# Optimization experiments

Measured on AMD Instinct MI355X. Metric: run time of the kernel, lower is better.

Reference implementation:

```python
import jax, jax.numpy as jnp
import numpy as np

N_NODES = 100000
N_EDGES = 1000000
NODE_DIM = 128
EDGE_DIM = 16
HID = 128


def _linear_init(key, fan_in, fan_out):
    # torch nn.Linear default: U(-1/sqrt(fan_in), 1/sqrt(fan_in))
    kw, kb = jax.random.split(key)
    bound = 1.0 / np.sqrt(fan_in)
    W = jax.random.uniform(kw, (fan_in, fan_out), jnp.float32, -bound, bound)
    b = jax.random.uniform(kb, (fan_out,), jnp.float32, -bound, bound)
    return W, b


def setup_inputs() -> dict:
    key = jax.random.key(0)
    ks = jax.random.split(key, 12)
    node_features = jax.random.normal(ks[0], (N_NODES, NODE_DIM), jnp.float32)
    edge_index = jax.random.randint(ks[1], (2, N_EDGES), 0, N_NODES, jnp.int64 if jax.config.read('jax_enable_x64') else jnp.int32)
    edge_features = jax.random.normal(ks[2], (N_EDGES, EDGE_DIM), jnp.float32)
    Wn1, bn1 = _linear_init(ks[3], NODE_DIM, HID)
    Wn2, bn2 = _linear_init(ks[4], HID, HID)
    We1, be1 = _linear_init(ks[5], EDGE_DIM, HID)
    We2, be2 = _linear_init(ks[6], HID, HID)
    Wp1, bp1 = _linear_init(ks[7], HID * 3, HID)
    Wp2, bp2 = _linear_init(ks[8], HID, HID // 2)
    Wp3, bp3 = _linear_init(ks[9], HID // 2, 1)
    return dict(node_features=node_features, edge_index=edge_index, edge_features=edge_features,
                Wn1=Wn1, bn1=bn1, Wn2=Wn2, bn2=bn2,
                We1=We1, be1=be1, We2=We2, be2=be2,
                Wp1=Wp1, bp1=bp1, Wp2=Wp2, bp2=bp2, Wp3=Wp3, bp3=bp3)


def reference(node_features, edge_index, edge_features,
              Wn1, bn1, Wn2, bn2, We1, be1, We2, be2,
              Wp1, bp1, Wp2, bp2, Wp3, bp3):
    # node/edge encoders: Linear -> ReLU -> Linear
    node_emb = jax.nn.relu(node_features @ Wn1 + bn1) @ Wn2 + bn2  # [N, H]
    edge_emb = jax.nn.relu(edge_features @ We1 + be1) @ We2 + be2  # [E, H]
    src = node_emb[edge_index[0]]  # [E, H] gather
    dst = node_emb[edge_index[1]]  # [E, H] gather
    combined = jnp.concatenate([src, dst, edge_emb], axis=1)  # [E, 3H]
    # predictor MLP (Dropout(0.2) is identity at inference)
    h = jax.nn.relu(combined @ Wp1 + bp1)
    h = jax.nn.relu(h @ Wp2 + bp2)
    scores = jax.nn.sigmoid(h @ Wp3 + bp3)  # [E, 1]
    return scores
```

## Files before the change

kernel.cpp:

```cpp
#include <hip/hip_runtime.h>

typedef _Float16 f16;
typedef _Float16 f16x8 __attribute__((ext_vector_type(8)));
typedef float    f32x4 __attribute__((ext_vector_type(4)));
typedef f16x8 f16x8_a __attribute__((may_alias));
typedef f16   f16_a   __attribute__((may_alias));

#define NN 100000
#define NE 1000000

static __device__ __forceinline__ f32x4 mfma16(f16x8 a, f16x8 b, f32x4 c) {
  return __builtin_amdgcn_mfma_f32_16x16x32_f16(a, b, c, 0, 0, 0);
}

static __device__ __forceinline__ f16x8 zero8() {
  f16x8 z; 
#pragma unroll
  for (int j = 0; j < 8; ++j) z[j] = (f16)0.f;
  return z;
}

template<int RB_LOG2, int SZ>
static __device__ __forceinline__ void load_weights(const f16* __restrict__ gw, char* lds) {
  const char* src = (const char*)gw;
#pragma unroll
  for (int g = threadIdx.x; g < SZ / 16; g += 256) {
    int byte = g << 4;
    int row  = byte >> RB_LOG2;
    int dstb = byte ^ ((row & 7) << 4);
    f16x8 v = *(const f16x8_a*)(src + byte);
    *(f16x8_a*)(lds + dstb) = v;
  }
}

template<int RB_LOG2>
static __device__ __forceinline__ f16x8 read_b(const char* lds, int n, int kbyte) {
  int byte = ((n << RB_LOG2) + kbyte) ^ ((n & 7) << 4);
  return *(const f16x8_a*)(lds + byte);
}

static __device__ __forceinline__ f16x8 act_read(const char* act, int base, int m, int kbyte) {
  int byte = (base + m * 256 + kbyte) ^ ((m & 7) << 4);
  return *(const f16x8_a*)(act + byte);
}

static __device__ __forceinline__ void act_write(char* act, int base, int m, int col, f16 v) {
  int byte = (base + m * 256 + col * 2) ^ ((m & 7) << 4);
  *(f16_a*)(act + byte) = v;
}

__global__ void transpose_w(const float* __restrict__ src, f16* __restrict__ dst,
                            int K, int N, int kOff, int ld) {
  int i = blockIdx.x * 256 + threadIdx.x;
  if (i >= N * K) return;
  int n = i / K, k = i - n * K;
  dst[i] = (f16)src[(size_t)(kOff + k) * ld + n];
}

__global__ __launch_bounds__(256, 2) void node_kernel(
    const float* __restrict__ nf, const f16* __restrict__ WnT1, const float* __restrict__ bn1,
    const f16* __restrict__ WnT2, const float* __restrict__ bn2, f16* __restrict__ emb) {
  __shared__ char wbuf[32768];
  __shared__ char act[32768];
  const int tid = threadIdx.x, w = tid >> 6, lane = tid & 63;
  const int c = lane & 15, kb = lane >> 4;
  const int base = blockIdx.x * 128 + w * 32;
  const int abase = w * 8192;

  load_weights<8, 32768>(WnT1, wbuf);
  __syncthreads();

  f16x8 a[2][4];
#pragma unroll
  for (int rt = 0; rt < 2; ++rt) {
    int r = base + rt * 16 + c; r = r < NN ? r : 0;
    const float* p = nf + (size_t)r * 128 + kb * 8;
#pragma unroll
    for (int ks = 0; ks < 4; ++ks) {
      float4 x0 = *(const float4*)(p + ks * 32);
      float4 x1 = *(const float4*)(p + ks * 32 + 4);
      f16x8 t;
      t[0]=(f16)x0.x; t[1]=(f16)x0.y; t[2]=(f16)x0.z; t[3]=(f16)x0.w;
      t[4]=(f16)x1.x; t[5]=(f16)x1.y; t[6]=(f16)x1.z; t[7]=(f16)x1.w;
      a[rt][ks] = t;
    }
  }

  f32x4 acc[2][8];
#pragma unroll
  for (int nt = 0; nt < 8; ++nt) {
    float bb = bn1[nt * 16 + c];
    acc[0][nt] = f32x4{bb, bb, bb, bb};
    acc[1][nt] = f32x4{bb, bb, bb, bb};
  }
#pragma unroll
  for (int ks = 0; ks < 4; ++ks)
#pragma unroll
    for (int nt = 0; nt < 8; ++nt) {
      f16x8 b = read_b<8>(wbuf, nt * 16 + c, ks * 64 + kb * 16);
      acc[0][nt] = mfma16(a[0][ks], b, acc[0][nt]);
      acc[1][nt] = mfma16(a[1][ks], b, acc[1][nt]);
    }
#pragma unroll
  for (int rt = 0; rt < 2; ++rt)
#pragma unroll
    for (int nt = 0; nt < 8; ++nt)
#pragma unroll
      for (int r = 0; r < 4; ++r) {
        float v = acc[rt][nt][r];
        v = v > 0.f ? v : 0.f;
        act_write(act, abase, rt * 16 + kb * 4 + r, nt * 16 + c, (f16)v);
      }

  __syncthreads();
  load_weights<8, 32768>(WnT2, wbuf);
  __syncthreads();

  f32x4 acc2[2][8];
#pragma unroll
  for (int nt = 0; nt < 8; ++nt) {
    float bb = bn2[nt * 16 + c];
    acc2[0][nt] = f32x4{bb, bb, bb, bb};
    acc2[1][nt] = f32x4{bb, bb, bb, bb};
  }
#pragma unroll
  for (int ks = 0; ks < 4; ++ks) {
    f16x8 a0 = act_read(act, abase, c,      ks * 64 + kb * 16);
    f16x8 a1 = act_read(act, abase, 16 + c, ks * 64 + kb * 16);
#pragma unroll
    for (int nt = 0; nt < 8; ++nt) {
      f16x8 b = read_b<8>(wbuf, nt * 16 + c, ks * 64 + kb * 16);
      acc2[0][nt] = mfma16(a0, b, acc2[0][nt]);
      acc2[1][nt] = mfma16(a1, b, acc2[1][nt]);
    }
  }
#pragma unroll
  for (int rt = 0; rt < 2; ++rt)
#pragma unroll
    for (int nt = 0; nt < 8; ++nt)
#pragma unroll
      for (int r = 0; r < 4; ++r) {
        int row = base + rt * 16 + kb * 4 + r;
        if (row < NN) emb[(size_t)row * 128 + nt * 16 + c] = (f16)acc2[rt][nt][r];
      }
}

__global__ __launch_bounds__(256, 2) void edge_kernel(
    const float* __restrict__ ef, const int* __restrict__ eidx,
    const f16* __restrict__ emb,
    const f16* __restrict__ WeT1, const float* __restrict__ be1,
    const f16* __restrict__ WeT2, const float* __restrict__ be2,
    const f16* __restrict__ Wp1a, const f16* __restrict__ Wp1b, const f16* __restrict__ Wp1c,
    const float* __restrict__ bp1,
    const f16* __restrict__ WpT2, const float* __restrict__ bp2,
    const float* __restrict__ Wp3, const float* __restrict__ bp3,
    float* __restrict__ out) {
  __shared__ char wbuf[32768];
  __shared__ char act[32768];
  const int tid = threadIdx.x, w = tid >> 6, lane = tid & 63;
  const int c = lane & 15, kb = lane >> 4;
  const int ebase = blockIdx.x * 128 + w * 32;
  const int abase = w * 8192;

  load_weights<5, 4096>(WeT1, wbuf);
  __syncthreads();
  {
    f16x8 a[2];
#pragma unroll
    for (int rt = 0; rt < 2; ++rt) {
      int m = ebase + rt * 16 + c; m = m < NE ? m : 0;
      f16x8 t = zero8();
      if (kb < 2) {
        const float* p = ef + (size_t)m * 16 + kb * 8;
        float4 x0 = *(const float4*)(p);
        float4 x1 = *(const float4*)(p + 4);
        t[0]=(f16)x0.x; t[1]=(f16)x0.y; t[2]=(f16)x0.z; t[3]=(f16)x0.w;
        t[4]=(f16)x1.x; t[5]=(f16)x1.y; t[6]=(f16)x1.z; t[7]=(f16)x1.w;
      }
      a[rt] = t;
    }
    f32x4 acc[2][8];
#pragma unroll
    for (int nt = 0; nt < 8; ++nt) {
      float bb = be1[nt * 16 + c];
      acc[0][nt] = f32x4{bb, bb, bb, bb};
      acc[1][nt] = f32x4{bb, bb, bb, bb};
    }
    int kbyte = (kb < 2) ? kb * 16 : 0;
#pragma unroll
    for (int nt = 0; nt < 8; ++nt) {
      f16x8 b = read_b<5>(wbuf, nt * 16 + c, kbyte);
      acc[0][nt] = mfma16(a[0], b, acc[0][nt]);
      acc[1][nt] = mfma16(a[1], b, acc[1][nt]);
    }
#pragma unroll
    for (int rt = 0; rt < 2; ++rt)
#pragma unroll
      for (int nt = 0; nt < 8; ++nt)
#pragma unroll
        for (int r = 0; r < 4; ++r) {
          float v = acc[rt][nt][r];
          v = v > 0.f ? v : 0.f;
          act_write(act, abase, rt * 16 + kb * 4 + r, nt * 16 + c, (f16)v);
        }
  }

  __syncthreads();
  load_weights<8, 32768>(WeT2, wbuf);
  __syncthreads();
  {
    f32x4 acc[2][8];
#pragma unroll
    for (int nt = 0; nt < 8; ++nt) {
      float bb = be2[nt * 16 + c];
      acc[0][nt] = f32x4{bb, bb, bb, bb};
      acc[1][nt] = f32x4{bb, bb, bb, bb};
    }
#pragma unroll
    for (int ks = 0; ks < 4; ++ks) {
      f16x8 a0 = act_read(act, abase, c,      ks * 64 + kb * 16);
      f16x8 a1 = act_read(act, abase, 16 + c, ks * 64 + kb * 16);
#pragma unroll
      for (int nt = 0; nt < 8; ++nt) {
        f16x8 b = read_b<8>(wbuf, nt * 16 + c, ks * 64 + kb * 16);
        acc[0][nt] = mfma16(a0, b, acc[0][nt]);
        acc[1][nt] = mfma16(a1, b, acc[1][nt]);
      }
    }
#pragma unroll
    for (int rt = 0; rt < 2; ++rt)
#pragma unroll
      for (int nt = 0; nt < 8; ++nt)
#pragma unroll
        for (int r = 0; r < 4; ++r)
          act_write(act, abase, rt * 16 + kb * 4 + r, nt * 16 + c, (f16)acc[rt][nt][r]);
  }

  f32x4 accp[2][8];
#pragma unroll
  for (int nt = 0; nt < 8; ++nt) {
    float bb = bp1[nt * 16 + c];
    accp[0][nt] = f32x4{bb, bb, bb, bb};
    accp[1][nt] = f32x4{bb, bb, bb, bb};
  }

  __syncthreads();
  load_weights<8, 32768>(Wp1a, wbuf);
  __syncthreads();
  {
    f16x8 a[2][4];
#pragma unroll
    for (int rt = 0; rt < 2; ++rt) {
      int m = ebase + rt * 16 + c; m = m < NE ? m : NE - 1;
      int s = eidx[m];
      const f16* np = emb + (size_t)s * 128 + kb * 8;
#pragma unroll
      for (int ks = 0; ks < 4; ++ks) a[rt][ks] = *(const f16x8_a*)(np + ks * 32);
    }
#pragma unroll
    for (int ks = 0; ks < 4; ++ks)
#pragma unroll
      for (int nt = 0; nt < 8; ++nt) {
        f16x8 b = read_b<8>(wbuf, nt * 16 + c, ks * 64 + kb * 16);
        accp[0][nt] = mfma16(a[0][ks], b, accp[0][nt]);
        accp[1][nt] = mfma16(a[1][ks], b, accp[1][nt]);
      }
  }

  __syncthreads();
  load_weights<8, 32768>(Wp1b, wbuf);
  __syncthreads();
  {
    f16x8 a[2][4];
#pragma unroll
    for (int rt = 0; rt < 2; ++rt) {
      int m = ebase + rt * 16 + c; m = m < NE ? m : NE - 1;
      int s = eidx[NE + m];
      const f16* np = emb + (size_t)s * 128 + kb * 8;
#pragma unroll
      for (int ks = 0; ks < 4; ++ks) a[rt][ks] = *(const f16x8_a*)(np + ks * 32);
    }
#pragma unroll
    for (int ks = 0; ks < 4; ++ks)
#pragma unroll
      for (int nt = 0; nt < 8; ++nt) {
        f16x8 b = read_b<8>(wbuf, nt * 16 + c, ks * 64 + kb * 16);
        accp[0][nt] = mfma16(a[0][ks], b, accp[0][nt]);
        accp[1][nt] = mfma16(a[1][ks], b, accp[1][nt]);
      }
  }

  __syncthreads();
  load_weights<8, 32768>(Wp1c, wbuf);
  __syncthreads();
  {
#pragma unroll
    for (int ks = 0; ks < 4; ++ks) {
      f16x8 a0 = act_read(act, abase, c,      ks * 64 + kb * 16);
      f16x8 a1 = act_read(act, abase, 16 + c, ks * 64 + kb * 16);
#pragma unroll
      for (int nt = 0; nt < 8; ++nt) {
        f16x8 b = read_b<8>(wbuf, nt * 16 + c, ks * 64 + kb * 16);
        accp[0][nt] = mfma16(a0, b, accp[0][nt]);
        accp[1][nt] = mfma16(a1, b, accp[1][nt]);
      }
    }
#pragma unroll
    for (int rt = 0; rt < 2; ++rt)
#pragma unroll
      for (int nt = 0; nt < 8; ++nt)
#pragma unroll
        for (int r = 0; r < 4; ++r) {
          float v = accp[rt][nt][r];
          v = v > 0.f ? v : 0.f;
          act_write(act, abase, rt * 16 + kb * 4 + r, nt * 16 + c, (f16)v);
        }
  }

  __syncthreads();
  load_weights<8, 16384>(WpT2, wbuf);
  __syncthreads();
  f32x4 accq[2][4];
#pragma unroll
  for (int nt = 0; nt < 4; ++nt) {
    float bb = bp2[nt * 16 + c];
    accq[0][nt] = f32x4{bb, bb, bb, bb};
    accq[1][nt] = f32x4{bb, bb, bb, bb};
  }
#pragma unroll
  for (int ks = 0; ks < 4; ++ks) {
    f16x8 a0 = act_read(act, abase, c,      ks * 64 + kb * 16);
    f16x8 a1 = act_read(act, abase, 16 + c, ks * 64 + kb * 16);
#pragma unroll
    for (int nt = 0; nt < 4; ++nt) {
      f16x8 b = read_b<8>(wbuf, nt * 16 + c, ks * 64 + kb * 16);
      accq[0][nt] = mfma16(a0, b, accq[0][nt]);
      accq[1][nt] = mfma16(a1, b, accq[1][nt]);
    }
  }

  float w3[4], b3 = bp3[0];
#pragma unroll
  for (int nt = 0; nt < 4; ++nt) w3[nt] = Wp3[nt * 16 + c];
#pragma unroll
  for (int rt = 0; rt < 2; ++rt) {
#pragma unroll
    for (int r = 0; r < 4; ++r) {
      float s = 0.f;
#pragma unroll
      for (int nt = 0; nt < 4; ++nt) {
        float h = accq[rt][nt][r];
        h = h > 0.f ? h : 0.f;
        s += h * w3[nt];
      }
      s += __shfl_xor(s, 1, 64);
      s += __shfl_xor(s, 2, 64);
      s += __shfl_xor(s, 4, 64);
      s += __shfl_xor(s, 8, 64);
      int m = ebase + rt * 16 + kb * 4 + r;
      if (c == r && m < NE) {
        out[m] = 1.f / (1.f + __expf(-(s + b3)));
      }
    }
  }
}

extern "C" void kernel_launch(void* const* d_in, const int* in_sizes, int n_in,
                              void* d_out, int out_size, void* d_ws, size_t ws_size,
                              hipStream_t stream) {
  const float* nf  = (const float*)d_in[0];
  const int*   ei  = (const int*)  d_in[1];
  const float* ef  = (const float*)d_in[2];
  const float* Wn1 = (const float*)d_in[3];
  const float* bn1 = (const float*)d_in[4];
  const float* Wn2 = (const float*)d_in[5];
  const float* bn2 = (const float*)d_in[6];
  const float* We1 = (const float*)d_in[7];
  const float* be1 = (const float*)d_in[8];
  const float* We2 = (const float*)d_in[9];
  const float* be2 = (const float*)d_in[10];
  const float* Wp1 = (const float*)d_in[11];
  const float* bp1 = (const float*)d_in[12];
  const float* Wp2 = (const float*)d_in[13];
  const float* bp2 = (const float*)d_in[14];
  const float* Wp3 = (const float*)d_in[15];
  const float* bp3 = (const float*)d_in[16];

  char* ws = (char*)d_ws;
  f16* WnT1 = (f16*)(ws);
  f16* WnT2 = (f16*)(ws + 32768);
  f16* WeT1 = (f16*)(ws + 65536);
  f16* WeT2 = (f16*)(ws + 69632);
  f16* Wp1a = (f16*)(ws + 102400);
  f16* Wp1b = (f16*)(ws + 135168);
  f16* Wp1c = (f16*)(ws + 167936);
  f16* WpT2 = (f16*)(ws + 200704);
  f16* emb  = (f16*)(ws + 217088);

  transpose_w<<<64, 256, 0, stream>>>(Wn1, WnT1, 128, 128, 0, 128);
  transpose_w<<<64, 256, 0, stream>>>(Wn2, WnT2, 128, 128, 0, 128);
  transpose_w<<<8,  256, 0, stream>>>(We1, WeT1, 16,  128, 0, 128);
  transpose_w<<<64, 256, 0, stream>>>(We2, WeT2, 128, 128, 0, 128);
  transpose_w<<<64, 256, 0, stream>>>(Wp1, Wp1a, 128, 128, 0,   128);
  transpose_w<<<64, 256, 0, stream>>>(Wp1, Wp1b, 128, 128, 128, 128);
  transpose_w<<<64, 256, 0, stream>>>(Wp1, Wp1c, 128, 128, 256, 128);
  transpose_w<<<32, 256, 0, stream>>>(Wp2, WpT2, 128, 64, 0, 64);

  node_kernel<<<782, 256, 0, stream>>>(nf, WnT1, bn1, WnT2, bn2, emb);
  edge_kernel<<<7813, 256, 0, stream>>>(ef, ei, emb, WeT1, be1, WeT2, be2,
                                        Wp1a, Wp1b, Wp1c, bp1, WpT2, bp2, Wp3, bp3,
                                        (float*)d_out);
}
```

Baseline: 485.1 us.

## Fold second-layer weights into predictor and precompute per-node projections

```diff
diff --git a/kernel.cpp b/kernel.cpp
--- a/kernel.cpp
+++ b/kernel.cpp
@@ -8,16 +8,26 @@
 
 #define NN 100000
 #define NE 1000000
+#define NT 31250
+#define EK_BLOCKS 512
+#define EK_WAVES (EK_BLOCKS * 4)
 
 static __device__ __forceinline__ f32x4 mfma16(f16x8 a, f16x8 b, f32x4 c) {
   return __builtin_amdgcn_mfma_f32_16x16x32_f16(a, b, c, 0, 0, 0);
 }
 
 static __device__ __forceinline__ f16x8 zero8() {
-  f16x8 z; 
+  f16x8 z;
 #pragma unroll
   for (int j = 0; j < 8; ++j) z[j] = (f16)0.f;
   return z;
+}
+
+static __device__ __forceinline__ f16x8 relu8(f16x8 x) {
+  f16x8 r;
+#pragma unroll
+  for (int j = 0; j < 8; ++j) r[j] = x[j] > (f16)0.f ? x[j] : (f16)0.f;
+  return r;
 }
 
 template<int RB_LOG2, int SZ>
@@ -57,9 +67,34 @@
   dst[i] = (f16)src[(size_t)(kOff + k) * ld + n];
 }
 
+__global__ void mm_fold(const float* __restrict__ A, const float* __restrict__ Wp1,
+                        int rowOff, f16* __restrict__ dstT) {
+  int g = blockIdx.x * 256 + threadIdx.x;
+  int i = g >> 7, j = g & 127;
+  float s = 0.f;
+#pragma unroll 8
+  for (int k = 0; k < 128; ++k) s += A[i * 128 + k] * Wp1[(size_t)(rowOff + k) * 128 + j];
+  dstT[j * 128 + i] = (f16)s;
+}
+
+__global__ void bias_fold(const float* __restrict__ bp1, const float* __restrict__ bn2,
+                          const float* __restrict__ be2, const float* __restrict__ Wp1,
+                          float* __restrict__ bfold) {
+  int j = threadIdx.x;
+  float s = bp1[j];
+#pragma unroll 8
+  for (int k = 0; k < 128; ++k)
+    s += bn2[k] * (Wp1[(size_t)k * 128 + j] + Wp1[(size_t)(128 + k) * 128 + j]);
+#pragma unroll 8
+  for (int k = 0; k < 128; ++k)
+    s += be2[k] * Wp1[(size_t)(256 + k) * 128 + j];
+  bfold[j] = s;
+}
+
 __global__ __launch_bounds__(256, 2) void node_kernel(
     const float* __restrict__ nf, const f16* __restrict__ WnT1, const float* __restrict__ bn1,
-    const f16* __restrict__ WnT2, const float* __restrict__ bn2, f16* __restrict__ emb) {
+    const f16* __restrict__ Wn2aT, const f16* __restrict__ Wn2bT, const float* __restrict__ bfold,
+    f16* __restrict__ PA, f16* __restrict__ PB) {
   __shared__ char wbuf[32768];
   __shared__ char act[32768];
   const int tid = threadIdx.x, w = tid >> 6, lane = tid & 63;
@@ -70,129 +105,37 @@
   load_weights<8, 32768>(WnT1, wbuf);
   __syncthreads();
 
-  f16x8 a[2][4];
-#pragma unroll
-  for (int rt = 0; rt < 2; ++rt) {
-    int r = base + rt * 16 + c; r = r < NN ? r : 0;
-    const float* p = nf + (size_t)r * 128 + kb * 8;
-#pragma unroll
-    for (int ks = 0; ks < 4; ++ks) {
-      float4 x0 = *(const float4*)(p + ks * 32);
-      float4 x1 = *(const float4*)(p + ks * 32 + 4);
-      f16x8 t;
-      t[0]=(f16)x0.x; t[1]=(f16)x0.y; t[2]=(f16)x0.z; t[3]=(f16)x0.w;
-      t[4]=(f16)x1.x; t[5]=(f16)x1.y; t[6]=(f16)x1.z; t[7]=(f16)x1.w;
-      a[rt][ks] = t;
-    }
-  }
-
-  f32x4 acc[2][8];
-#pragma unroll
-  for (int nt = 0; nt < 8; ++nt) {
-    float bb = bn1[nt * 16 + c];
-    acc[0][nt] = f32x4{bb, bb, bb, bb};
-    acc[1][nt] = f32x4{bb, bb, bb, bb};
-  }
-#pragma unroll
-  for (int ks = 0; ks < 4; ++ks)
-#pragma unroll
-    for (int nt = 0; nt < 8; ++nt) {
-      f16x8 b = read_b<8>(wbuf, nt * 16 + c, ks * 64 + kb * 16);
-      acc[0][nt] = mfma16(a[0][ks], b, acc[0][nt]);
-      acc[1][nt] = mfma16(a[1][ks], b, acc[1][nt]);
-    }
-#pragma unroll
-  for (int rt = 0; rt < 2; ++rt)
-#pragma unroll
-    for (int nt = 0; nt < 8; ++nt)
-#pragma unroll
-      for (int r = 0; r < 4; ++r) {
-        float v = acc[rt][nt][r];
-        v = v > 0.f ? v : 0.f;
-        act_write(act, abase, rt * 16 + kb * 4 + r, nt * 16 + c, (f16)v);
-      }
-
-  __syncthreads();
-  load_weights<8, 32768>(WnT2, wbuf);
-  __syncthreads();
-
-  f32x4 acc2[2][8];
-#pragma unroll
-  for (int nt = 0; nt < 8; ++nt) {
-    float bb = bn2[nt * 16 + c];
-    acc2[0][nt] = f32x4{bb, bb, bb, bb};
-    acc2[1][nt] = f32x4{bb, bb, bb, bb};
-  }
-#pragma unroll
-  for (int ks = 0; ks < 4; ++ks) {
-    f16x8 a0 = act_read(act, abase, c,      ks * 64 + kb * 16);
-    f16x8 a1 = act_read(act, abase, 16 + c, ks * 64 + kb * 16);
-#pragma unroll
-    for (int nt = 0; nt < 8; ++nt) {
-      f16x8 b = read_b<8>(wbuf, nt * 16 + c, ks * 64 + kb * 16);
-      acc2[0][nt] = mfma16(a0, b, acc2[0][nt]);
-      acc2[1][nt] = mfma16(a1, b, acc2[1][nt]);
-    }
-  }
-#pragma unroll
-  for (int rt = 0; rt < 2; ++rt)
-#pragma unroll
-    for (int nt = 0; nt < 8; ++nt)
-#pragma unroll
-      for (int r = 0; r < 4; ++r) {
-        int row = base + rt * 16 + kb * 4 + r;
-        if (row < NN) emb[(size_t)row * 128 + nt * 16 + c] = (f16)acc2[rt][nt][r];
-      }
-}
-
-__global__ __launch_bounds__(256, 2) void edge_kernel(
-    const float* __restrict__ ef, const int* __restrict__ eidx,
-    const f16* __restrict__ emb,
-    const f16* __restrict__ WeT1, const float* __restrict__ be1,
-    const f16* __restrict__ WeT2, const float* __restrict__ be2,
-    const f16* __restrict__ Wp1a, const f16* __restrict__ Wp1b, const f16* __restrict__ Wp1c,
-    const float* __restrict__ bp1,
-    const f16* __restrict__ WpT2, const float* __restrict__ bp2,
-    const float* __restrict__ Wp3, const float* __restrict__ bp3,
-    float* __restrict__ out) {
-  __shared__ char wbuf[32768];
-  __shared__ char act[32768];
-  const int tid = threadIdx.x, w = tid >> 6, lane = tid & 63;
-  const int c = lane & 15, kb = lane >> 4;
-  const int ebase = blockIdx.x * 128 + w * 32;
-  const int abase = w * 8192;
-
-  load_weights<5, 4096>(WeT1, wbuf);
-  __syncthreads();
   {
-    f16x8 a[2];
+    f16x8 a[2][4];
 #pragma unroll
     for (int rt = 0; rt < 2; ++rt) {
-      int m = ebase + rt * 16 + c; m = m < NE ? m : 0;
-      f16x8 t = zero8();
-      if (kb < 2) {
-        const float* p = ef + (size_t)m * 16 + kb * 8;
-        float4 x0 = *(const float4*)(p);
-        float4 x1 = *(const float4*)(p + 4);
+      int r = base + rt * 16 + c; r = r < NN ? r : 0;
+      const float* p = nf + (size_t)r * 128 + kb * 8;
+#pragma unroll
+      for (int ks = 0; ks < 4; ++ks) {
+        float4 x0 = *(const float4*)(p + ks * 32);
+        float4 x1 = *(const float4*)(p + ks * 32 + 4);
+        f16x8 t;
         t[0]=(f16)x0.x; t[1]=(f16)x0.y; t[2]=(f16)x0.z; t[3]=(f16)x0.w;
         t[4]=(f16)x1.x; t[5]=(f16)x1.y; t[6]=(f16)x1.z; t[7]=(f16)x1.w;
-      }
-      a[rt] = t;
+        a[rt][ks] = t;
+      }
     }
     f32x4 acc[2][8];
 #pragma unroll
     for (int nt = 0; nt < 8; ++nt) {
-      float bb = be1[nt * 16 + c];
+      float bb = bn1[nt * 16 + c];
       acc[0][nt] = f32x4{bb, bb, bb, bb};
       acc[1][nt] = f32x4{bb, bb, bb, bb};
     }
-    int kbyte = (kb < 2) ? kb * 16 : 0;
-#pragma unroll
-    for (int nt = 0; nt < 8; ++nt) {
-      f16x8 b = read_b<5>(wbuf, nt * 16 + c, kbyte);
-      acc[0][nt] = mfma16(a[0], b, acc[0][nt]);
-      acc[1][nt] = mfma16(a[1], b, acc[1][nt]);
-    }
+#pragma unroll
+    for (int ks = 0; ks < 4; ++ks)
+#pragma unroll
+      for (int nt = 0; nt < 8; ++nt) {
+        f16x8 b = read_b<8>(wbuf, nt * 16 + c, ks * 64 + kb * 16);
+        acc[0][nt] = mfma16(a[0][ks], b, acc[0][nt]);
+        acc[1][nt] = mfma16(a[1][ks], b, acc[1][nt]);
+      }
 #pragma unroll
     for (int rt = 0; rt < 2; ++rt)
 #pragma unroll
@@ -206,13 +149,13 @@
   }
 
   __syncthreads();
-  load_weights<8, 32768>(WeT2, wbuf);
+  load_weights<8, 32768>(Wn2aT, wbuf);
   __syncthreads();
   {
     f32x4 acc[2][8];
 #pragma unroll
     for (int nt = 0; nt < 8; ++nt) {
-      float bb = be2[nt * 16 + c];
+      float bb = bfold[nt * 16 + c];
       acc[0][nt] = f32x4{bb, bb, bb, bb};
       acc[1][nt] = f32x4{bb, bb, bb, bb};
     }
@@ -232,68 +175,22 @@
 #pragma unroll
       for (int nt = 0; nt < 8; ++nt)
 #pragma unroll
-        for (int r = 0; r < 4; ++r)
-          act_write(act, abase, rt * 16 + kb * 4 + r, nt * 16 + c, (f16)acc[rt][nt][r]);
-  }
-
-  f32x4 accp[2][8];
-#pragma unroll
-  for (int nt = 0; nt < 8; ++nt) {
-    float bb = bp1[nt * 16 + c];
-    accp[0][nt] = f32x4{bb, bb, bb, bb};
-    accp[1][nt] = f32x4{bb, bb, bb, bb};
-  }
-
-  __syncthreads();
-  load_weights<8, 32768>(Wp1a, wbuf);
+        for (int r = 0; r < 4; ++r) {
+          int row = base + rt * 16 + kb * 4 + r;
+          if (row < NN) PA[(size_t)row * 128 + nt * 16 + c] = (f16)acc[rt][nt][r];
+        }
+  }
+
+  __syncthreads();
+  load_weights<8, 32768>(Wn2bT, wbuf);
   __syncthreads();
   {
-    f16x8 a[2][4];
-#pragma unroll
-    for (int rt = 0; rt < 2; ++rt) {
-      int m = ebase + rt * 16 + c; m = m < NE ? m : NE - 1;
-      int s = eidx[m];
-      const f16* np = emb + (size_t)s * 128 + kb * 8;
-#pragma unroll
-      for (int ks = 0; ks < 4; ++ks) a[rt][ks] = *(const f16x8_a*)(np + ks * 32);
-    }
-#pragma unroll
-    for (int ks = 0; ks < 4; ++ks)
-#pragma unroll
-      for (int nt = 0; nt < 8; ++nt) {
-        f16x8 b = read_b<8>(wbuf, nt * 16 + c, ks * 64 + kb * 16);
-        accp[0][nt] = mfma16(a[0][ks], b, accp[0][nt]);
-        accp[1][nt] = mfma16(a[1][ks], b, accp[1][nt]);
-      }
-  }
-
-  __syncthreads();
-  load_weights<8, 32768>(Wp1b, wbuf);
-  __syncthreads();
-  {
-    f16x8 a[2][4];
-#pragma unroll
-    for (int rt = 0; rt < 2; ++rt) {
-      int m = ebase + rt * 16 + c; m = m < NE ? m : NE - 1;
-      int s = eidx[NE + m];
-      const f16* np = emb + (size_t)s * 128 + kb * 8;
-#pragma unroll
-      for (int ks = 0; ks < 4; ++ks) a[rt][ks] = *(const f16x8_a*)(np + ks * 32);
-    }
-#pragma unroll
-    for (int ks = 0; ks < 4; ++ks)
-#pragma unroll
-      for (int nt = 0; nt < 8; ++nt) {
-        f16x8 b = read_b<8>(wbuf, nt * 16 + c, ks * 64 + kb * 16);
-        accp[0][nt] = mfma16(a[0][ks], b, accp[0][nt]);
-        accp[1][nt] = mfma16(a[1][ks], b, accp[1][nt]);
-      }
-  }
-
-  __syncthreads();
-  load_weights<8, 32768>(Wp1c, wbuf);
-  __syncthreads();
-  {
+    f32x4 acc[2][8];
+#pragma unroll
+    for (int nt = 0; nt < 8; ++nt) {
+      acc[0][nt] = f32x4{0.f, 0.f, 0.f, 0.f};
+      acc[1][nt] = f32x4{0.f, 0.f, 0.f, 0.f};
+    }
 #pragma unroll
     for (int ks = 0; ks < 4; ++ks) {
       f16x8 a0 = act_read(act, abase, c,      ks * 64 + kb * 16);
@@ -301,8 +198,8 @@
 #pragma unroll
       for (int nt = 0; nt < 8; ++nt) {
         f16x8 b = read_b<8>(wbuf, nt * 16 + c, ks * 64 + kb * 16);
-        accp[0][nt] = mfma16(a0, b, accp[0][nt]);
-        accp[1][nt] = mfma16(a1, b, accp[1][nt]);
+        acc[0][nt] = mfma16(a0, b, acc[0][nt]);
+        acc[1][nt] = mfma16(a1, b, acc[1][nt]);
       }
     }
 #pragma unroll
@@ -311,55 +208,171 @@
       for (int nt = 0; nt < 8; ++nt)
 #pragma unroll
         for (int r = 0; r < 4; ++r) {
-          float v = accp[rt][nt][r];
-          v = v > 0.f ? v : 0.f;
-          act_write(act, abase, rt * 16 + kb * 4 + r, nt * 16 + c, (f16)v);
-        }
-  }
-
-  __syncthreads();
-  load_weights<8, 16384>(WpT2, wbuf);
-  __syncthreads();
-  f32x4 accq[2][4];
-#pragma unroll
-  for (int nt = 0; nt < 4; ++nt) {
-    float bb = bp2[nt * 16 + c];
-    accq[0][nt] = f32x4{bb, bb, bb, bb};
-    accq[1][nt] = f32x4{bb, bb, bb, bb};
-  }
-#pragma unroll
-  for (int ks = 0; ks < 4; ++ks) {
-    f16x8 a0 = act_read(act, abase, c,      ks * 64 + kb * 16);
-    f16x8 a1 = act_read(act, abase, 16 + c, ks * 64 + kb * 16);
+          int row = base + rt * 16 + kb * 4 + r;
+          if (row < NN) PB[(size_t)row * 128 + nt * 16 + c] = (f16)acc[rt][nt][r];
+        }
+  }
+}
+
+__global__ __launch_bounds__(256, 2) void edge_kernel(
+    const float* __restrict__ ef, const int* __restrict__ eidx,
+    const f16* __restrict__ WeT1, const float* __restrict__ be1,
+    const f16* __restrict__ WCT, const f16* __restrict__ WpT2g,
+    const float* __restrict__ bp2, const float* __restrict__ Wp3, const float* __restrict__ bp3,
+    const f16* __restrict__ PA, const f16* __restrict__ PB,
+    float* __restrict__ out) {
+  __shared__ char wc[32768];
+  __shared__ char wp2[16384];
+  __shared__ char act[32768];
+  const int tid = threadIdx.x, w = tid >> 6, lane = tid & 63;
+  const int c = lane & 15, kb = lane >> 4;
+  const int abase = w * 8192;
+
+  load_weights<8, 32768>(WCT, wc);
+  load_weights<8, 16384>(WpT2g, wp2);
+  __syncthreads();
+
+  f16x8 w1frag[8];
+  float bias_e1[8], bias_p2[4], w3[4];
+#pragma unroll
+  for (int nt = 0; nt < 8; ++nt) {
+    w1frag[nt] = *(const f16x8_a*)(WeT1 + (nt * 16 + c) * 16 + (kb & 1) * 8);
+    bias_e1[nt] = be1[nt * 16 + c];
+  }
+#pragma unroll
+  for (int nt = 0; nt < 4; ++nt) { bias_p2[nt] = bp2[nt * 16 + c]; w3[nt] = Wp3[nt * 16 + c]; }
+  const float b3 = bp3[0];
+
+  const int gw = blockIdx.x * 4 + w;
+  for (int t = gw; t < NT; t += EK_WAVES) {
+    const int ebase = t * 32;
+    const int e0 = ebase + c, e1 = e0 + 16;
+    const int s0 = eidx[e0],      s1 = eidx[e1];
+    const int d0 = eidx[NE + e0], d1 = eidx[NE + e1];
+
+    f16x8 gpa0[4], gpa1[4], gpb0[4], gpb1[4];
+    {
+      const f16* p0 = PA + (size_t)s0 * 128 + kb * 8;
+      const f16* p1 = PA + (size_t)s1 * 128 + kb * 8;
+      const f16* q0 = PB + (size_t)d0 * 128 + kb * 8;
+      const f16* q1 = PB + (size_t)d1 * 128 + kb * 8;
+#pragma unroll
+      for (int ks = 0; ks < 4; ++ks) {
+        gpa0[ks] = *(const f16x8_a*)(p0 + ks * 32);
+        gpa1[ks] = *(const f16x8_a*)(p1 + ks * 32);
+        gpb0[ks] = *(const f16x8_a*)(q0 + ks * 32);
+        gpb1[ks] = *(const f16x8_a*)(q1 + ks * 32);
+      }
+    }
+
+    {
+      f16x8 ae[2];
+#pragma unroll
+      for (int rt = 0; rt < 2; ++rt) {
+        f16x8 v = zero8();
+        if (kb < 2) {
+          const float* p = ef + (size_t)(ebase + rt * 16 + c) * 16 + kb * 8;
+          float4 x0 = *(const float4*)(p);
+          float4 x1 = *(const float4*)(p + 4);
+          v[0]=(f16)x0.x; v[1]=(f16)x0.y; v[2]=(f16)x0.z; v[3]=(f16)x0.w;
+          v[4]=(f16)x1.x; v[5]=(f16)x1.y; v[6]=(f16)x1.z; v[7]=(f16)x1.w;
+        }
+        ae[rt] = v;
+      }
+      f32x4 acc[2][8];
+#pragma unroll
+      for (int nt = 0; nt < 8; ++nt) {
+        acc[0][nt] = f32x4{bias_e1[nt], bias_e1[nt], bias_e1[nt], bias_e1[nt]};
+        acc[1][nt] = acc[0][nt];
+      }
+#pragma unroll
+      for (int nt = 0; nt < 8; ++nt) {
+        acc[0][nt] = mfma16(ae[0], w1frag[nt], acc[0][nt]);
+        acc[1][nt] = mfma16(ae[1], w1frag[nt], acc[1][nt]);
+      }
+#pragma unroll
+      for (int rt = 0; rt < 2; ++rt)
+#pragma unroll
+        for (int nt = 0; nt < 8; ++nt)
+#pragma unroll
+          for (int r = 0; r < 4; ++r) {
+            float v = acc[rt][nt][r];
+            v = v > 0.f ? v : 0.f;
+            act_write(act, abase, rt * 16 + kb * 4 + r, nt * 16 + c, (f16)v);
+          }
+    }
+
+    {
+      f32x4 acc[2][8];
+#pragma unroll
+      for (int nt = 0; nt < 8; ++nt) {
+        acc[0][nt] = f32x4{0.f, 0.f, 0.f, 0.f};
+        acc[1][nt] = f32x4{0.f, 0.f, 0.f, 0.f};
+      }
+#pragma unroll
+      for (int ks = 0; ks < 4; ++ks) {
+        f16x8 a0 = act_read(act, abase, c,      ks * 64 + kb * 16);
+        f16x8 a1 = act_read(act, abase, 16 + c, ks * 64 + kb * 16);
+#pragma unroll
+        for (int nt = 0; nt < 8; ++nt) {
+          f16x8 b = read_b<8>(wc, nt * 16 + c, ks * 64 + kb * 16);
+          acc[0][nt] = mfma16(a0, b, acc[0][nt]);
+          acc[1][nt] = mfma16(a1, b, acc[1][nt]);
+        }
+      }
+#pragma unroll
+      for (int rt = 0; rt < 2; ++rt)
+#pragma unroll
+        for (int nt = 0; nt < 8; ++nt)
+#pragma unroll
+          for (int r = 0; r < 4; ++r)
+            act_write(act, abase, rt * 16 + kb * 4 + r, nt * 16 + c, (f16)acc[rt][nt][r]);
+    }
+
+    f32x4 accq[2][4];
 #pragma unroll
     for (int nt = 0; nt < 4; ++nt) {
-      f16x8 b = read_b<8>(wbuf, nt * 16 + c, ks * 64 + kb * 16);
-      accq[0][nt] = mfma16(a0, b, accq[0][nt]);
-      accq[1][nt] = mfma16(a1, b, accq[1][nt]);
-    }
-  }
-
-  float w3[4], b3 = bp3[0];
-#pragma unroll
-  for (int nt = 0; nt < 4; ++nt) w3[nt] = Wp3[nt * 16 + c];
-#pragma unroll
-  for (int rt = 0; rt < 2; ++rt) {
-#pragma unroll
-    for (int r = 0; r < 4; ++r) {
-      float s = 0.f;
-#pragma unroll
-      for (int nt = 0; nt < 4; ++nt) {
-        float h = accq[rt][nt][r];
-        h = h > 0.f ? h : 0.f;
-        s += h * w3[nt];
-      }
-      s += __shfl_xor(s, 1, 64);
-      s += __shfl_xor(s, 2, 64);
-      s += __shfl_xor(s, 4, 64);
-      s += __shfl_xor(s, 8, 64);
-      int m = ebase + rt * 16 + kb * 4 + r;
-      if (c == r && m < NE) {
-        out[m] = 1.f / (1.f + __expf(-(s + b3)));
+      accq[0][nt] = f32x4{bias_p2[nt], bias_p2[nt], bias_p2[nt], bias_p2[nt]};
+      accq[1][nt] = accq[0][nt];
+    }
+    {
+      f16x8 ap0[4], ap1[4];
+#pragma unroll
+      for (int ks = 0; ks < 4; ++ks) {
+        f16x8 x0 = act_read(act, abase, c,      ks * 64 + kb * 16);
+        f16x8 x1 = act_read(act, abase, 16 + c, ks * 64 + kb * 16);
+        ap0[ks] = relu8(x0 + gpa0[ks] + gpb0[ks]);
+        ap1[ks] = relu8(x1 + gpa1[ks] + gpb1[ks]);
+      }
+#pragma unroll
+      for (int ks = 0; ks < 4; ++ks)
+#pragma unroll
+        for (int nt = 0; nt < 4; ++nt) {
+          f16x8 b = read_b<8>(wp2, nt * 16 + c, ks * 64 + kb * 16);
+          accq[0][nt] = mfma16(ap0[ks], b, accq[0][nt]);
+          accq[1][nt] = mfma16(ap1[ks], b, accq[1][nt]);
+        }
+    }
+
+#pragma unroll
+    for (int rt = 0; rt < 2; ++rt) {
+#pragma unroll
+      for (int r = 0; r < 4; ++r) {
+        float s = 0.f;
+#pragma unroll
+        for (int nt = 0; nt < 4; ++nt) {
+          float h = accq[rt][nt][r];
+          h = h > 0.f ? h : 0.f;
+          s += h * w3[nt];
+        }
+        s += __shfl_xor(s, 1, 64);
+        s += __shfl_xor(s, 2, 64);
+        s += __shfl_xor(s, 4, 64);
+        s += __shfl_xor(s, 8, 64);
+        int m = ebase + rt * 16 + kb * 4 + r;
+        if (c == r) {
+          out[m] = 1.f / (1.f + __expf(-(s + b3)));
+        }
       }
     }
   }
@@ -387,27 +400,25 @@
   const float* bp3 = (const float*)d_in[16];
 
   char* ws = (char*)d_ws;
-  f16* WnT1 = (f16*)(ws);
-  f16* WnT2 = (f16*)(ws + 32768);
-  f16* WeT1 = (f16*)(ws + 65536);
-  f16* WeT2 = (f16*)(ws + 69632);
-  f16* Wp1a = (f16*)(ws + 102400);
-  f16* Wp1b = (f16*)(ws + 135168);
-  f16* Wp1c = (f16*)(ws + 167936);
-  f16* WpT2 = (f16*)(ws + 200704);
-  f16* emb  = (f16*)(ws + 217088);
+  f16*   WnT1  = (f16*)(ws);
+  f16*   Wn2aT = (f16*)(ws + 32768);
+  f16*   Wn2bT = (f16*)(ws + 65536);
+  f16*   WeT1  = (f16*)(ws + 98304);
+  f16*   WCT   = (f16*)(ws + 102400);
+  f16*   WpT2  = (f16*)(ws + 135168);
+  float* bfold = (float*)(ws + 151552);
+  f16*   PA    = (f16*)(ws + 155648);
+  f16*   PB    = (f16*)(ws + 155648 + 25600000);
 
   transpose_w<<<64, 256, 0, stream>>>(Wn1, WnT1, 128, 128, 0, 128);
-  transpose_w<<<64, 256, 0, stream>>>(Wn2, WnT2, 128, 128, 0, 128);
   transpose_w<<<8,  256, 0, stream>>>(We1, WeT1, 16,  128, 0, 128);
-  transpose_w<<<64, 256, 0, stream>>>(We2, WeT2, 128, 128, 0, 128);
-  transpose_w<<<64, 256, 0, stream>>>(Wp1, Wp1a, 128, 128, 0,   128);
-  transpose_w<<<64, 256, 0, stream>>>(Wp1, Wp1b, 128, 128, 128, 128);
-  transpose_w<<<64, 256, 0, stream>>>(Wp1, Wp1c, 128, 128, 256, 128);
   transpose_w<<<32, 256, 0, stream>>>(Wp2, WpT2, 128, 64, 0, 64);
-
-  node_kernel<<<782, 256, 0, stream>>>(nf, WnT1, bn1, WnT2, bn2, emb);
-  edge_kernel<<<7813, 256, 0, stream>>>(ef, ei, emb, WeT1, be1, WeT2, be2,
-                                        Wp1a, Wp1b, Wp1c, bp1, WpT2, bp2, Wp3, bp3,
-                                        (float*)d_out);
-}
+  mm_fold<<<64, 256, 0, stream>>>(Wn2, Wp1, 0,   Wn2aT);
+  mm_fold<<<64, 256, 0, stream>>>(Wn2, Wp1, 128, Wn2bT);
+  mm_fold<<<64, 256, 0, stream>>>(We2, Wp1, 256, WCT);
+  bias_fold<<<1, 128, 0, stream>>>(bp1, bn2, be2, Wp1, bfold);
+
+  node_kernel<<<782, 256, 0, stream>>>(nf, WnT1, bn1, Wn2aT, Wn2bT, bfold, PA, PB);
+  edge_kernel<<<EK_BLOCKS, 256, 0, stream>>>(ef, ei, WeT1, be1, WCT, WpT2,
+                                             bp2, Wp3, bp3, PA, PB, (float*)d_out);
+}
```

Result: slower. 625.2 us (+28.9%).
